# Optimization experiments

Hardware: AMD Instinct MI355X
Metric: run time of the kernel (lower is better)

## Reference

```python
import jax, jax.numpy as jnp
import numpy as np

B, S, D, H = 2, 2048, 1024, 16
HD = D // H  # head dim = 64


def setup_inputs() -> dict:
    key = jax.random.key(0)
    ks = jax.random.split(key, 5)
    scale = 1.0 / np.sqrt(D)
    return {
        "hidden_states": jax.random.normal(ks[0], (B, S, D), jnp.float32),
        "attention_mask": jax.random.normal(ks[1], (B, 1, 1, S), jnp.float32),
        "Wq": jax.random.normal(ks[2], (D, D), jnp.float32) * scale,
        "bq": jnp.zeros((D,), jnp.float32),
        "Wk": jax.random.normal(ks[3], (D, D), jnp.float32) * scale,
        "bk": jnp.zeros((D,), jnp.float32),
        "Wv": jax.random.normal(ks[4], (D, D), jnp.float32) * scale,
        "bv": jnp.zeros((D,), jnp.float32),
    }


def _split_heads(x):
    # [B,S,D] -> [B,H,S,HD]
    return x.reshape(B, S, H, HD).transpose(0, 2, 1, 3)


def reference(hidden_states, attention_mask, Wq, bq, Wk, bk, Wv, bv):
    # torch Linear: y = x @ W.T + b
    q = _split_heads(hidden_states @ Wq.T + bq)
    k = _split_heads(hidden_states @ Wk.T + bk)
    v = _split_heads(hidden_states @ Wv.T + bv)

    scores = jnp.einsum("bhqd,bhkd->bhqk", q, k)
    # Faithful to source: with a mask present, the 1/sqrt(head_dim) scaling
    # is overwritten and raw scores are multiplied by the binary key mask.
    mask = (attention_mask >= 0).astype(scores.dtype)  # [B,1,1,S]
    probs = scores * mask
    # dropout prob = 0 (eval) -> identity

    ctx = jnp.einsum("bhqk,bhkd->bhqd", probs, v)
    ctx = ctx.transpose(0, 2, 1, 3).reshape(B, S, D)
    return ctx
```

## Files before the change

### kernel.cpp

```cpp
#include <hip/hip_runtime.h>

#define BB 2
#define SS 2048
#define DD 1024
#define HH 16
#define HDIM 64
#define MTOT 4096

typedef unsigned short u16;
typedef __bf16 bf16_t;
typedef bf16_t bf16x8 __attribute__((ext_vector_type(8)));
typedef float floatx4 __attribute__((ext_vector_type(4)));

__device__ __forceinline__ float bf2f(u16 u) {
  union { unsigned int i; float f; } x;
  x.i = ((unsigned int)u) << 16;
  return x.f;
}
__device__ __forceinline__ u16 f2bf(float f) {
  union { float f; unsigned int i; } x;
  x.f = f;
  unsigned int r = x.i + 0x7fffu + ((x.i >> 16) & 1u);
  return (u16)(r >> 16);
}

__global__ __launch_bounds__(256) void cast_to_bf16(
    const float* __restrict__ hs, const float* __restrict__ wq,
    const float* __restrict__ wk, const float* __restrict__ wv,
    u16* __restrict__ hs_b, u16* __restrict__ wq_b,
    u16* __restrict__ wk_b, u16* __restrict__ wv_b) {
  int fid = blockIdx.x * 256 + threadIdx.x;
  const float* src;
  u16* dst;
  int local;
  if (fid < 1048576) { src = hs; dst = hs_b; local = fid; }
  else if (fid < 1310720) { src = wq; dst = wq_b; local = fid - 1048576; }
  else if (fid < 1572864) { src = wk; dst = wk_b; local = fid - 1310720; }
  else { src = wv; dst = wv_b; local = fid - 1572864; }
  float4 v = reinterpret_cast<const float4*>(src)[local];
  ushort4 o;
  o.x = f2bf(v.x); o.y = f2bf(v.y); o.z = f2bf(v.z); o.w = f2bf(v.w);
  reinterpret_cast<ushort4*>(dst)[local] = o;
}

#define BKK 32
#define LDT 40
__global__ __launch_bounds__(256) void qkv_gemm_kernel(
    const u16* __restrict__ A,
    const u16* __restrict__ Wq, const u16* __restrict__ Wk, const u16* __restrict__ Wv,
    const float* __restrict__ bq, const float* __restrict__ bk, const float* __restrict__ bv,
    u16* __restrict__ Qo, u16* __restrict__ Ko, u16* __restrict__ Vo) {
  __shared__ u16 sA[128 * LDT];
  __shared__ u16 sB[128 * LDT];
  const int mt = blockIdx.y, ntall = blockIdx.x;
  const int seg = ntall >> 3, nt = ntall & 7;
  const u16* Wp = (seg == 0) ? Wq : (seg == 1) ? Wk : Wv;
  const float* bp = (seg == 0) ? bq : (seg == 1) ? bk : bv;
  u16* Out = (seg == 0) ? Qo : (seg == 1) ? Ko : Vo;
  const int m0 = mt * 128, n0 = nt * 128;
  const int tid = threadIdx.x;
  const int lane = tid & 63, wave = tid >> 6;
  const int wm = (wave >> 1) * 64, wn = (wave & 1) * 64;
  const int quad = lane >> 4, l16 = lane & 15;
  floatx4 acc[4][4] = {};
  for (int k0 = 0; k0 < DD; k0 += BKK) {
#pragma unroll
    for (int c = 0; c < 2; ++c) {
      int L = tid + c * 256;
      int row = L >> 2;
      int col = (L & 3) * 8;
      *reinterpret_cast<uint4*>(sA + row * LDT + col) =
          *reinterpret_cast<const uint4*>(A + (size_t)(m0 + row) * DD + k0 + col);
      *reinterpret_cast<uint4*>(sB + row * LDT + col) =
          *reinterpret_cast<const uint4*>(Wp + (size_t)(n0 + row) * DD + k0 + col);
    }
    __syncthreads();
    bf16x8 af[4], bfr[4];
#pragma unroll
    for (int i = 0; i < 4; ++i) {
      af[i]  = *reinterpret_cast<const bf16x8*>(sA + (wm + i * 16 + l16) * LDT + quad * 8);
      bfr[i] = *reinterpret_cast<const bf16x8*>(sB + (wn + i * 16 + l16) * LDT + quad * 8);
    }
#pragma unroll
    for (int i = 0; i < 4; ++i)
#pragma unroll
      for (int j = 0; j < 4; ++j)
        acc[i][j] = __builtin_amdgcn_mfma_f32_16x16x32_bf16(af[i], bfr[j], acc[i][j], 0, 0, 0);
    __syncthreads();
  }
#pragma unroll
  for (int j = 0; j < 4; ++j) {
    int col = n0 + wn + j * 16 + l16;
    float bias = bp[col];
#pragma unroll
    for (int i = 0; i < 4; ++i) {
#pragma unroll
      for (int r = 0; r < 4; ++r) {
        int row = m0 + wm + i * 16 + quad * 4 + r;
        Out[(size_t)row * DD + col] = f2bf(acc[i][j][r] + bias);
      }
    }
  }
}

__global__ __launch_bounds__(256) void m_partial_kernel(
    const u16* __restrict__ Kb, const u16* __restrict__ Vb,
    const float* __restrict__ am, float* __restrict__ Mpart) {
  __shared__ float sK[64 * 68];
  __shared__ float sV[64 * 68];
  const int chunk = blockIdx.x;
  const int bh = blockIdx.y;
  const int b = bh >> 4, h = bh & 15;
  const int s0 = chunk * 64;
  const int tid = threadIdx.x;
#pragma unroll
  for (int c = 0; c < 2; ++c) {
    int L = tid + c * 256;
    int srow = L >> 3;
    int col = (L & 7) * 8;
    size_t g = (size_t)(b * SS + s0 + srow) * DD + h * HDIM + col;
    uint4 kraw = *reinterpret_cast<const uint4*>(Kb + g);
    uint4 vraw = *reinterpret_cast<const uint4*>(Vb + g);
    float m = (am[b * SS + s0 + srow] >= 0.f) ? 1.f : 0.f;
    unsigned int kw[4] = {kraw.x, kraw.y, kraw.z, kraw.w};
    unsigned int vw[4] = {vraw.x, vraw.y, vraw.z, vraw.w};
#pragma unroll
    for (int q = 0; q < 4; ++q) {
      sK[srow * 68 + col + 2 * q]     = m * bf2f((u16)(kw[q] & 0xffffu));
      sK[srow * 68 + col + 2 * q + 1] = m * bf2f((u16)(kw[q] >> 16));
      sV[srow * 68 + col + 2 * q]     = bf2f((u16)(vw[q] & 0xffffu));
      sV[srow * 68 + col + 2 * q + 1] = bf2f((u16)(vw[q] >> 16));
    }
  }
  __syncthreads();
  const int e0 = (tid & 15) * 4, d0 = (tid >> 4) * 4;
  float acc[4][4] = {};
  for (int s = 0; s < 64; ++s) {
    float4 kk = *reinterpret_cast<const float4*>(&sK[s * 68 + e0]);
    float4 vv = *reinterpret_cast<const float4*>(&sV[s * 68 + d0]);
    float ka[4] = {kk.x, kk.y, kk.z, kk.w};
    float va[4] = {vv.x, vv.y, vv.z, vv.w};
#pragma unroll
    for (int i = 0; i < 4; ++i)
#pragma unroll
      for (int j = 0; j < 4; ++j) acc[i][j] += ka[i] * va[j];
  }
  float* outp = Mpart + ((size_t)(chunk * 32 + bh)) * 4096;
#pragma unroll
  for (int i = 0; i < 4; ++i) {
    float4 o = {acc[i][0], acc[i][1], acc[i][2], acc[i][3]};
    *reinterpret_cast<float4*>(&outp[(e0 + i) * 64 + d0]) = o;
  }
}

__global__ __launch_bounds__(256) void m_reduce_kernel(
    const float* __restrict__ Mpart, float* __restrict__ M) {
  int idx = blockIdx.x * 256 + threadIdx.x;
  int bh = idx >> 12, ed = idx & 4095;
  float s = 0.f;
#pragma unroll
  for (int c = 0; c < 32; ++c) s += Mpart[((size_t)(c * 32 + bh) << 12) + ed];
  M[idx] = s;
}

__global__ __launch_bounds__(256) void ctx_kernel(
    const u16* __restrict__ Qb, const float* __restrict__ M, float* __restrict__ Out) {
  __shared__ float sM[64 * 68];
  __shared__ float sQ[64 * 68];
  const int mchunk = blockIdx.x;
  const int h = blockIdx.y;
  const int m0 = mchunk * 64;
  const int b = m0 >> 11;
  const int bh = b * HH + h;
  const int tid = threadIdx.x;
  const float* Mp = M + (size_t)bh * 4096;
#pragma unroll
  for (int c = 0; c < 16; ++c) {
    int L = c * 256 + tid;
    int e = L >> 6, d = L & 63;
    sM[e * 68 + d] = Mp[L];
  }
#pragma unroll
  for (int c = 0; c < 2; ++c) {
    int L = tid + c * 256;
    int row = L >> 3, col = (L & 7) * 8;
    uint4 q = *reinterpret_cast<const uint4*>(Qb + (size_t)(m0 + row) * DD + h * HDIM + col);
    unsigned int w[4] = {q.x, q.y, q.z, q.w};
#pragma unroll
    for (int t = 0; t < 4; ++t) {
      sQ[row * 68 + col + 2 * t]     = bf2f((u16)(w[t] & 0xffffu));
      sQ[row * 68 + col + 2 * t + 1] = bf2f((u16)(w[t] >> 16));
    }
  }
  __syncthreads();
  const int d0 = (tid & 15) * 4, ml0 = (tid >> 4) * 4;
  float acc[4][4] = {};
  for (int e = 0; e < 64; ++e) {
    float4 mm = *reinterpret_cast<const float4*>(&sM[e * 68 + d0]);
    float ma[4] = {mm.x, mm.y, mm.z, mm.w};
#pragma unroll
    for (int i = 0; i < 4; ++i) {
      float qv = sQ[(ml0 + i) * 68 + e];
#pragma unroll
      for (int j = 0; j < 4; ++j) acc[i][j] += qv * ma[j];
    }
  }
#pragma unroll
  for (int i = 0; i < 4; ++i) {
    float4 o = {acc[i][0], acc[i][1], acc[i][2], acc[i][3]};
    *reinterpret_cast<float4*>(Out + (size_t)(m0 + ml0 + i) * DD + h * HDIM + d0) = o;
  }
}

extern "C" void kernel_launch(void* const* d_in, const int* in_sizes, int n_in,
                              void* d_out, int out_size, void* d_ws, size_t ws_size,
                              hipStream_t stream) {
  const float* hs = (const float*)d_in[0];
  const float* am = (const float*)d_in[1];
  const float* wq = (const float*)d_in[2];
  const float* bq = (const float*)d_in[3];
  const float* wk = (const float*)d_in[4];
  const float* bk = (const float*)d_in[5];
  const float* wv = (const float*)d_in[6];
  const float* bv = (const float*)d_in[7];
  float* out = (float*)d_out;
  char* ws = (char*)d_ws;

  u16* hs_b = (u16*)(ws);
  u16* wq_b = (u16*)(ws + 8388608);
  u16* wk_b = (u16*)(ws + 10485760);
  u16* wv_b = (u16*)(ws + 12582912);
  u16* q_b  = (u16*)(ws + 14680064);
  u16* k_b  = (u16*)(ws + 23068672);
  u16* v_b  = (u16*)(ws + 31457280);
  float* mpart = (float*)(ws + 39845888);
  float* mfull = (float*)(ws + 56623104);

  cast_to_bf16<<<7168, 256, 0, stream>>>(hs, wq, wk, wv, hs_b, wq_b, wk_b, wv_b);
  qkv_gemm_kernel<<<dim3(24, 32), 256, 0, stream>>>(hs_b, wq_b, wk_b, wv_b,
                                                    bq, bk, bv, q_b, k_b, v_b);
  m_partial_kernel<<<dim3(32, 32), 256, 0, stream>>>(k_b, v_b, am, mpart);
  m_reduce_kernel<<<512, 256, 0, stream>>>(mpart, mfull);
  ctx_kernel<<<dim3(64, 16), 256, 0, stream>>>(q_b, mfull, out);
}
```

Baseline: 162.6 us.

## Use direct global-to-LDS loads in GEMM, atomic M reduction, vectorized ctx loop

After: 163.2 us. About the same (+0.4%).

```diff
diff --git a/kernel.cpp b/kernel.cpp
--- a/kernel.cpp
+++ b/kernel.cpp
@@ -24,12 +24,25 @@
   return (u16)(r >> 16);
 }
 
+__device__ __forceinline__ void gload16(const u16* g, u16* l) {
+  __builtin_amdgcn_global_load_lds(
+      (const __attribute__((address_space(1))) unsigned int*)g,
+      (__attribute__((address_space(3))) unsigned int*)l, 16, 0, 0);
+}
+
 __global__ __launch_bounds__(256) void cast_to_bf16(
     const float* __restrict__ hs, const float* __restrict__ wq,
     const float* __restrict__ wk, const float* __restrict__ wv,
     u16* __restrict__ hs_b, u16* __restrict__ wq_b,
-    u16* __restrict__ wk_b, u16* __restrict__ wv_b) {
+    u16* __restrict__ wk_b, u16* __restrict__ wv_b,
+    float* __restrict__ mfull) {
   int fid = blockIdx.x * 256 + threadIdx.x;
+  if (fid >= 1835008) {
+    int z = fid - 1835008;
+    float4 zero = {0.f, 0.f, 0.f, 0.f};
+    reinterpret_cast<float4*>(mfull)[z] = zero;
+    return;
+  }
   const float* src;
   u16* dst;
   int local;
@@ -44,14 +57,13 @@
 }
 
 #define BKK 32
-#define LDT 40
 __global__ __launch_bounds__(256) void qkv_gemm_kernel(
     const u16* __restrict__ A,
     const u16* __restrict__ Wq, const u16* __restrict__ Wk, const u16* __restrict__ Wv,
     const float* __restrict__ bq, const float* __restrict__ bk, const float* __restrict__ bv,
     u16* __restrict__ Qo, u16* __restrict__ Ko, u16* __restrict__ Vo) {
-  __shared__ u16 sA[128 * LDT];
-  __shared__ u16 sB[128 * LDT];
+  __shared__ u16 sA[128 * BKK];
+  __shared__ u16 sB[128 * BKK];
   const int mt = blockIdx.y, ntall = blockIdx.x;
   const int seg = ntall >> 3, nt = ntall & 7;
   const u16* Wp = (seg == 0) ? Wq : (seg == 1) ? Wk : Wv;
@@ -62,24 +74,22 @@
   const int lane = tid & 63, wave = tid >> 6;
   const int wm = (wave >> 1) * 64, wn = (wave & 1) * 64;
   const int quad = lane >> 4, l16 = lane & 15;
+  const int srow0 = wave * 32 + (lane >> 2);
+  const int scol = (lane & 3) * 8;
   floatx4 acc[4][4] = {};
   for (int k0 = 0; k0 < DD; k0 += BKK) {
 #pragma unroll
     for (int c = 0; c < 2; ++c) {
-      int L = tid + c * 256;
-      int row = L >> 2;
-      int col = (L & 3) * 8;
-      *reinterpret_cast<uint4*>(sA + row * LDT + col) =
-          *reinterpret_cast<const uint4*>(A + (size_t)(m0 + row) * DD + k0 + col);
-      *reinterpret_cast<uint4*>(sB + row * LDT + col) =
-          *reinterpret_cast<const uint4*>(Wp + (size_t)(n0 + row) * DD + k0 + col);
+      int r = srow0 + c * 16;
+      gload16(A + (size_t)(m0 + r) * DD + k0 + scol, sA + r * BKK + scol);
+      gload16(Wp + (size_t)(n0 + r) * DD + k0 + scol, sB + r * BKK + scol);
     }
     __syncthreads();
     bf16x8 af[4], bfr[4];
 #pragma unroll
     for (int i = 0; i < 4; ++i) {
-      af[i]  = *reinterpret_cast<const bf16x8*>(sA + (wm + i * 16 + l16) * LDT + quad * 8);
-      bfr[i] = *reinterpret_cast<const bf16x8*>(sB + (wn + i * 16 + l16) * LDT + quad * 8);
+      af[i]  = *reinterpret_cast<const bf16x8*>(sA + (wm + i * 16 + l16) * BKK + quad * 8);
+      bfr[i] = *reinterpret_cast<const bf16x8*>(sB + (wn + i * 16 + l16) * BKK + quad * 8);
     }
 #pragma unroll
     for (int i = 0; i < 4; ++i)
@@ -105,62 +115,54 @@
 
 __global__ __launch_bounds__(256) void m_partial_kernel(
     const u16* __restrict__ Kb, const u16* __restrict__ Vb,
-    const float* __restrict__ am, float* __restrict__ Mpart) {
+    const float* __restrict__ am, float* __restrict__ mfull) {
   __shared__ float sK[64 * 68];
   __shared__ float sV[64 * 68];
-  const int chunk = blockIdx.x;
   const int bh = blockIdx.y;
   const int b = bh >> 4, h = bh & 15;
-  const int s0 = chunk * 64;
   const int tid = threadIdx.x;
-#pragma unroll
-  for (int c = 0; c < 2; ++c) {
-    int L = tid + c * 256;
-    int srow = L >> 3;
-    int col = (L & 7) * 8;
-    size_t g = (size_t)(b * SS + s0 + srow) * DD + h * HDIM + col;
-    uint4 kraw = *reinterpret_cast<const uint4*>(Kb + g);
-    uint4 vraw = *reinterpret_cast<const uint4*>(Vb + g);
-    float m = (am[b * SS + s0 + srow] >= 0.f) ? 1.f : 0.f;
-    unsigned int kw[4] = {kraw.x, kraw.y, kraw.z, kraw.w};
-    unsigned int vw[4] = {vraw.x, vraw.y, vraw.z, vraw.w};
-#pragma unroll
-    for (int q = 0; q < 4; ++q) {
-      sK[srow * 68 + col + 2 * q]     = m * bf2f((u16)(kw[q] & 0xffffu));
-      sK[srow * 68 + col + 2 * q + 1] = m * bf2f((u16)(kw[q] >> 16));
-      sV[srow * 68 + col + 2 * q]     = bf2f((u16)(vw[q] & 0xffffu));
-      sV[srow * 68 + col + 2 * q + 1] = bf2f((u16)(vw[q] >> 16));
-    }
-  }
-  __syncthreads();
   const int e0 = (tid & 15) * 4, d0 = (tid >> 4) * 4;
   float acc[4][4] = {};
-  for (int s = 0; s < 64; ++s) {
-    float4 kk = *reinterpret_cast<const float4*>(&sK[s * 68 + e0]);
-    float4 vv = *reinterpret_cast<const float4*>(&sV[s * 68 + d0]);
-    float ka[4] = {kk.x, kk.y, kk.z, kk.w};
-    float va[4] = {vv.x, vv.y, vv.z, vv.w};
-#pragma unroll
-    for (int i = 0; i < 4; ++i)
-#pragma unroll
-      for (int j = 0; j < 4; ++j) acc[i][j] += ka[i] * va[j];
-  }
-  float* outp = Mpart + ((size_t)(chunk * 32 + bh)) * 4096;
-#pragma unroll
-  for (int i = 0; i < 4; ++i) {
-    float4 o = {acc[i][0], acc[i][1], acc[i][2], acc[i][3]};
-    *reinterpret_cast<float4*>(&outp[(e0 + i) * 64 + d0]) = o;
-  }
-}
-
-__global__ __launch_bounds__(256) void m_reduce_kernel(
-    const float* __restrict__ Mpart, float* __restrict__ M) {
-  int idx = blockIdx.x * 256 + threadIdx.x;
-  int bh = idx >> 12, ed = idx & 4095;
-  float s = 0.f;
-#pragma unroll
-  for (int c = 0; c < 32; ++c) s += Mpart[((size_t)(c * 32 + bh) << 12) + ed];
-  M[idx] = s;
+  for (int cs = 0; cs < 2; ++cs) {
+    const int s0 = (blockIdx.x * 2 + cs) * 64;
+    if (cs) __syncthreads();
+#pragma unroll
+    for (int c = 0; c < 2; ++c) {
+      int L = tid + c * 256;
+      int srow = L >> 3;
+      int col = (L & 7) * 8;
+      size_t g = (size_t)(b * SS + s0 + srow) * DD + h * HDIM + col;
+      uint4 kraw = *reinterpret_cast<const uint4*>(Kb + g);
+      uint4 vraw = *reinterpret_cast<const uint4*>(Vb + g);
+      float m = (am[b * SS + s0 + srow] >= 0.f) ? 1.f : 0.f;
+      unsigned int kw[4] = {kraw.x, kraw.y, kraw.z, kraw.w};
+      unsigned int vw[4] = {vraw.x, vraw.y, vraw.z, vraw.w};
+#pragma unroll
+      for (int q = 0; q < 4; ++q) {
+        sK[srow * 68 + col + 2 * q]     = m * bf2f((u16)(kw[q] & 0xffffu));
+        sK[srow * 68 + col + 2 * q + 1] = m * bf2f((u16)(kw[q] >> 16));
+        sV[srow * 68 + col + 2 * q]     = bf2f((u16)(vw[q] & 0xffffu));
+        sV[srow * 68 + col + 2 * q + 1] = bf2f((u16)(vw[q] >> 16));
+      }
+    }
+    __syncthreads();
+    for (int s = 0; s < 64; ++s) {
+      float4 kk = *reinterpret_cast<const float4*>(&sK[s * 68 + e0]);
+      float4 vv = *reinterpret_cast<const float4*>(&sV[s * 68 + d0]);
+      float ka[4] = {kk.x, kk.y, kk.z, kk.w};
+      float va[4] = {vv.x, vv.y, vv.z, vv.w};
+#pragma unroll
+      for (int i = 0; i < 4; ++i)
+#pragma unroll
+        for (int j = 0; j < 4; ++j) acc[i][j] += ka[i] * va[j];
+    }
+  }
+  float* outp = mfull + (size_t)bh * 4096;
+#pragma unroll
+  for (int i = 0; i < 4; ++i)
+#pragma unroll
+    for (int j = 0; j < 4; ++j)
+      atomicAdd(&outp[(e0 + i) * 64 + d0 + j], acc[i][j]);
 }
 
 __global__ __launch_bounds__(256) void ctx_kernel(
@@ -195,15 +197,27 @@
   __syncthreads();
   const int d0 = (tid & 15) * 4, ml0 = (tid >> 4) * 4;
   float acc[4][4] = {};
-  for (int e = 0; e < 64; ++e) {
-    float4 mm = *reinterpret_cast<const float4*>(&sM[e * 68 + d0]);
-    float ma[4] = {mm.x, mm.y, mm.z, mm.w};
-#pragma unroll
-    for (int i = 0; i < 4; ++i) {
-      float qv = sQ[(ml0 + i) * 68 + e];
-#pragma unroll
-      for (int j = 0; j < 4; ++j) acc[i][j] += qv * ma[j];
-    }
+  for (int e4 = 0; e4 < 64; e4 += 4) {
+    float4 mm[4], qq[4];
+#pragma unroll
+    for (int t = 0; t < 4; ++t)
+      mm[t] = *reinterpret_cast<const float4*>(&sM[(e4 + t) * 68 + d0]);
+#pragma unroll
+    for (int i = 0; i < 4; ++i)
+      qq[i] = *reinterpret_cast<const float4*>(&sQ[(ml0 + i) * 68 + e4]);
+    float ma[4][4], qa[4][4];
+#pragma unroll
+    for (int t = 0; t < 4; ++t) {
+      ma[t][0] = mm[t].x; ma[t][1] = mm[t].y; ma[t][2] = mm[t].z; ma[t][3] = mm[t].w;
+      qa[t][0] = qq[t].x; qa[t][1] = qq[t].y; qa[t][2] = qq[t].z; qa[t][3] = qq[t].w;
+    }
+#pragma unroll
+    for (int i = 0; i < 4; ++i)
+#pragma unroll
+      for (int t = 0; t < 4; ++t)
+#pragma unroll
+        for (int j = 0; j < 4; ++j)
+          acc[i][j] += qa[i][t] * ma[t][j];
   }
 #pragma unroll
   for (int i = 0; i < 4; ++i) {
@@ -233,13 +247,11 @@
   u16* q_b  = (u16*)(ws + 14680064);
   u16* k_b  = (u16*)(ws + 23068672);
   u16* v_b  = (u16*)(ws + 31457280);
-  float* mpart = (float*)(ws + 39845888);
-  float* mfull = (float*)(ws + 56623104);
-
-  cast_to_bf16<<<7168, 256, 0, stream>>>(hs, wq, wk, wv, hs_b, wq_b, wk_b, wv_b);
+  float* mfull = (float*)(ws + 39845888);
+
+  cast_to_bf16<<<7296, 256, 0, stream>>>(hs, wq, wk, wv, hs_b, wq_b, wk_b, wv_b, mfull);
   qkv_gemm_kernel<<<dim3(24, 32), 256, 0, stream>>>(hs_b, wq_b, wk_b, wv_b,
                                                     bq, bk, bv, q_b, k_b, v_b);
-  m_partial_kernel<<<dim3(32, 32), 256, 0, stream>>>(k_b, v_b, am, mpart);
-  m_reduce_kernel<<<512, 256, 0, stream>>>(mpart, mfull);
+  m_partial_kernel<<<dim3(16, 32), 256, 0, stream>>>(k_b, v_b, am, mfull);
   ctx_kernel<<<dim3(64, 16), 256, 0, stream>>>(q_b, mfull, out);
 }
```
